# Performance work log

Measured on AMD Instinct MI355X. Metric: run time of the kernel, lower is better.

Reference implementation:

```python
import jax, jax.numpy as jnp
import numpy as np

N_PER_CLOUD = 2048   # points per cloud (batch entries are equal-sized, sorted)
NUM_CLOUDS = 8       # batch_size constant in the source module
RADIUS = 0.2         # init arg r
MAX_NEIGHBORS = 32   # init arg max_neighbors
F_IN, H1, H2, F_OUT = 3, 64, 64, 128  # PointNet++ SA MLP widths; nn input = F_IN + 3


def setup_inputs() -> dict:
    key = jax.random.key(0)
    ks = jax.random.split(key, 8)
    N = NUM_CLOUDS * N_PER_CLOUD
    x = jax.random.normal(ks[0], (N, F_IN), dtype=jnp.float32)
    pos = jax.random.uniform(ks[1], (N, 3), dtype=jnp.float32)  # unit cube
    batch = jnp.repeat(jnp.arange(NUM_CLOUDS, dtype=jnp.int32), N_PER_CLOUD)
    d_in = F_IN + 3
    W1 = jax.random.normal(ks[2], (d_in, H1), dtype=jnp.float32) / np.sqrt(d_in)
    b1 = jnp.zeros((H1,), dtype=jnp.float32)
    W2 = jax.random.normal(ks[3], (H1, H2), dtype=jnp.float32) / np.sqrt(H1)
    b2 = jnp.zeros((H2,), dtype=jnp.float32)
    W3 = jax.random.normal(ks[4], (H2, F_OUT), dtype=jnp.float32) / np.sqrt(H2)
    b3 = jnp.zeros((F_OUT,), dtype=jnp.float32)
    return dict(x=x, pos=pos, batch=batch, W1=W1, b1=b1, W2=W2, b2=b2, W3=W3, b3=b3)


def reference(x, pos, batch, W1, b1, W2, b2, W3, b3):
    N = pos.shape[0]
    B = N // N_PER_CLOUD
    n = N_PER_CLOUD
    posb = pos.reshape(B, n, 3)
    xb = x.reshape(B, n, -1)

    # --- radius ball query (per cloud, first MAX_NEIGHBORS in index order) ---
    diff = posb[:, :, None, :] - posb[:, None, :, :]          # [B, n_query, n_src, 3]
    d2 = jnp.sum(diff * diff, axis=-1)                        # [B, n, n]
    valid = d2 <= RADIUS * RADIUS                             # includes self -> >=1 nbr
    j_idx = jnp.arange(n, dtype=jnp.int32)
    keys = jnp.where(valid, j_idx[None, None, :], n)          # invalid -> sentinel n
    nbr = jnp.argsort(keys, axis=-1)[..., :MAX_NEIGHBORS]     # [B, n, K]
    nbr_ok = jnp.take_along_axis(keys, nbr, axis=-1) < n      # [B, n, K] bool

    # --- PointNetConv: msg = nn(cat([x_j, pos_j - pos_i])), max aggregation ---
    b_ix = jnp.arange(B)[:, None, None]
    x_j = xb[b_ix, nbr]                                        # [B, n, K, F_IN]
    rel = posb[b_ix, nbr] - posb[:, :, None, :]               # [B, n, K, 3]
    msg = jnp.concatenate([x_j, rel], axis=-1)                # [B, n, K, F_IN+3]
    h = jax.nn.relu(msg @ W1 + b1)
    h = jax.nn.relu(h @ W2 + b2)
    h = h @ W3 + b3                                           # [B, n, K, F_OUT]
    h = jnp.where(nbr_ok[..., None], h, -jnp.inf)
    out = jnp.max(h, axis=2).reshape(N, -1)                   # [N, F_OUT]
    return out, pos, batch
```

## Files before the change

### kernel.cpp

```cpp
#include <hip/hip_runtime.h>
#include <hip/hip_bf16.h>
#include <math.h>

#define NPC   2048
#define NC    8
#define NTOT  (NPC * NC)
#define KMAX  32
#define R2    0.04f

typedef short bf16x8  __attribute__((ext_vector_type(8)));
typedef float f32x16  __attribute__((ext_vector_type(16)));

__device__ __forceinline__ unsigned int f2bf(float f) {
    unsigned int u = __float_as_uint(f);
    return (u + 0x7FFFu + ((u >> 16) & 1u)) >> 16;
}

__device__ __forceinline__ unsigned int pkbf(float a, float b) {
    unsigned int r;
    asm("v_cvt_pk_bf16_f32 %0, %1, %2" : "=v"(r) : "v"(a), "v"(b));
    return r;
}

__device__ __forceinline__ void epi_swap(const f32x16& a0, const f32x16& a1,
                                         int hi, bf16x8 bout[4]) {
    unsigned int w_own[2][4][2];
    #pragma unroll
    for (int g = 0; g < 4; ++g) {
        w_own[0][g][0] = pkbf(fmaxf(a0[4*g+0],0.f), fmaxf(a0[4*g+1],0.f));
        w_own[0][g][1] = pkbf(fmaxf(a0[4*g+2],0.f), fmaxf(a0[4*g+3],0.f));
        w_own[1][g][0] = pkbf(fmaxf(a1[4*g+0],0.f), fmaxf(a1[4*g+1],0.f));
        w_own[1][g][1] = pkbf(fmaxf(a1[4*g+2],0.f), fmaxf(a1[4*g+3],0.f));
    }
    unsigned int R[2][2][2];
    #pragma unroll
    for (int t = 0; t < 2; ++t)
        #pragma unroll
        for (int gg = 0; gg < 2; ++gg)
            #pragma unroll
            for (int u = 0; u < 2; ++u) {
                unsigned int send = hi ? w_own[t][2*gg][u] : w_own[t][2*gg+1][u];
                R[t][gg][u] = (unsigned int)__shfl_xor((int)send, 32);
            }
    #pragma unroll
    for (int kk = 0; kk < 4; ++kk) {
        int t = kk >> 1;
        unsigned int O0 = hi ? w_own[t][(2*kk+1)&3][0] : w_own[t][(2*kk)&3][0];
        unsigned int O1 = hi ? w_own[t][(2*kk+1)&3][1] : w_own[t][(2*kk)&3][1];
        unsigned int R0 = R[t][kk&1][0], R1 = R[t][kk&1][1];
        int4 w;
        w.x = (int)(hi ? R0 : O0);
        w.y = (int)(hi ? R1 : O1);
        w.z = (int)(hi ? O0 : R0);
        w.w = (int)(hi ? O1 : R1);
        bout[kk] = __builtin_bit_cast(bf16x8, w);
    }
}

__global__ __launch_bounds__(256) void prep_kernel(
    const float* __restrict__ x, const float* __restrict__ pos,
    const int* __restrict__ batch,
    const float* __restrict__ W1, const float* __restrict__ b1,
    const float* __restrict__ W2, const float* __restrict__ b2,
    const float* __restrict__ W3,
    int* __restrict__ nbr, int* __restrict__ cnts,
    float* __restrict__ xp, unsigned short* __restrict__ wf,
    float* __restrict__ out)
{
    int b = blockIdx.x, tid = threadIdx.x;
    if (b < 4096) {
        int q    = b * 4 + (tid >> 6);
        int lane = tid & 63;
        int base = (q >> 11) << 11;
        float qx = pos[3*q], qy = pos[3*q+1], qz = pos[3*q+2];
        int cnt = 0;
        for (int j0 = 0; j0 < NPC && cnt < KMAX; j0 += 256) {
            unsigned long long ms[4];
            bool vs[4];
            #pragma unroll
            for (int s = 0; s < 4; ++s) {
                int j = base + j0 + s*64 + lane;
                float dx = __fsub_rn(pos[3*j],   qx);
                float dy = __fsub_rn(pos[3*j+1], qy);
                float dz = __fsub_rn(pos[3*j+2], qz);
                float d2 = __fadd_rn(__fadd_rn(__fmul_rn(dx,dx), __fmul_rn(dy,dy)),
                                     __fmul_rn(dz,dz));
                vs[s] = d2 <= R2;
                ms[s] = __ballot(vs[s]);
            }
            #pragma unroll
            for (int s = 0; s < 4; ++s) {
                int before = (int)__popcll(ms[s] & ((1ull << lane) - 1ull));
                int slot = cnt + before;
                if (vs[s] && slot < KMAX) nbr[(q << 5) + slot] = base + j0 + s*64 + lane;
                cnt += (int)__popcll(ms[s]);
            }
        }
        if (lane == 0) cnts[q] = cnt < KMAX ? cnt : KMAX;
    } else if (b < 4160) {
        int i = (b - 4096) * 256 + tid;
        float4 v0 = {x[3*i], x[3*i+1], x[3*i+2], pos[3*i]};
        float4 v1 = {pos[3*i+1], pos[3*i+2], 0.f, 0.f};
        float4* dst = (float4*)(xp + 8 * i);
        dst[0] = v0; dst[1] = v1;
    } else if (b < 4216) {
        int g = (b - 4160) * 256 + tid;
        if (g < 1024) {
            int j = g & 7, lane = (g >> 3) & 63, t = g >> 9;
            int k = (lane >> 5)*8 + j, ch = t*32 + (lane & 31);
            float v = (k < 6) ? W1[k*64 + ch] : (k == 6 ? b1[ch] : 0.f);
            wf[g] = (unsigned short)f2bf(v);
        } else if (g < 6144) {
            int g2 = g - 1024;
            int j = g2 & 7, lane = (g2 >> 3) & 63, f = g2 >> 9;
            int t = f / 5, kk = f % 5;
            int k = kk*16 + (lane >> 5)*8 + j, row = t*32 + (lane & 31);
            float v = 0.f;
            if (k < 64)       v = W2[k*64 + row];
            else if (k == 64) v = b2[row];
            wf[g] = (unsigned short)f2bf(v);
        } else {
            int g3 = g - 6144;
            int j = g3 & 7, lane = (g3 >> 3) & 63, f = g3 >> 9;
            int n = f >> 2, kk = f & 3;
            int k = kk*16 + (lane >> 5)*8 + j, col = n*32 + (lane & 31);
            wf[g] = (unsigned short)f2bf(W3[k*128 + col]);
        }
    } else {
        int i = (b - 4216) * 256 + tid;
        if (i < NTOT*3) out[NTOT*128 + i] = pos[i];
        if (i < NTOT)   out[NTOT*131 + i] = (float)batch[i];
    }
}

__global__ __launch_bounds__(256, 4) void mlp_kernel(
    const unsigned short* __restrict__ wf, const float* __restrict__ b3,
    const float* __restrict__ xp,
    const int* __restrict__ nbr, const int* __restrict__ cnts,
    float* __restrict__ out)
{
    __shared__ int4 sW[1664];

    const int tid = threadIdx.x;
    const int4* wsrc = (const int4*)(wf + 1024);
    #pragma unroll
    for (int it = 0; it < 7; ++it) {
        int idx = it*256 + tid;
        if (idx < 1664) sW[idx] = wsrc[idx];
    }
    const int lane = tid & 63, wave = tid >> 6;
    const int e = lane & 31, hi = lane >> 5;
    bf16x8 wf1_0 = *(const bf16x8*)(wf + (0*64 + lane)*8);
    bf16x8 wf1_1 = *(const bf16x8*)(wf + (1*64 + lane)*8);
    __syncthreads();

    const unsigned int one_w = pkbf(1.0f, 0.0f);
    int4 ow = {0,0,0,0};
    if (!hi) ow.x = (int)one_w;
    const bf16x8 onef = __builtin_bit_cast(bf16x8, ow);

    float b3v0 = b3[0*32 + e], b3v1 = b3[1*32 + e], b3v2 = b3[2*32 + e], b3v3 = b3[3*32 + e];

    const int qbase = __builtin_amdgcn_readfirstlane(blockIdx.x * 16 + wave * 4);

    #pragma unroll 1
    for (int i = 0; i < 4; ++i) {
        const int qq = qbase + i;
        const int cnt = cnts[qq];

        int jg = (e < cnt) ? nbr[(qq << 5) + e] : qq;
        const float4* pj = (const float4*)(xp + 8*jg);
        float4 xj0 = pj[0], xj1 = pj[1];
        const float4* pq = (const float4*)(xp + 8*qq);
        float4 xq0 = pq[0], xq1 = pq[1];
        float r0 = xj0.w - xq0.w, r1 = xj1.x - xq1.x, r2 = xj1.y - xq1.y;

        int4 mw;
        mw.x = hi ? 0 : (int)pkbf(xj0.x, xj0.y);
        mw.y = hi ? 0 : (int)pkbf(xj0.z, r0);
        mw.z = hi ? 0 : (int)pkbf(r1, r2);
        mw.w = hi ? 0 : (int)one_w;
        bf16x8 msgf = __builtin_bit_cast(bf16x8, mw);

        f32x16 acc0 = {}, acc1 = {};
        acc0 = __builtin_amdgcn_mfma_f32_32x32x16_bf16(wf1_0, msgf, acc0, 0, 0, 0);
        acc1 = __builtin_amdgcn_mfma_f32_32x32x16_bf16(wf1_1, msgf, acc1, 0, 0, 0);
        bf16x8 h1f[4];
        epi_swap(acc0, acc1, hi, h1f);

        f32x16 c20 = {}, c21 = {};
        #pragma unroll
        for (int kk = 0; kk < 4; ++kk) {
            c20 = __builtin_amdgcn_mfma_f32_32x32x16_bf16(
                    *(const bf16x8*)&sW[(0*5 + kk)*64 + lane], h1f[kk], c20, 0, 0, 0);
            c21 = __builtin_amdgcn_mfma_f32_32x32x16_bf16(
                    *(const bf16x8*)&sW[(1*5 + kk)*64 + lane], h1f[kk], c21, 0, 0, 0);
        }
        c20 = __builtin_amdgcn_mfma_f32_32x32x16_bf16(
                *(const bf16x8*)&sW[(0*5 + 4)*64 + lane], onef, c20, 0, 0, 0);
        c21 = __builtin_amdgcn_mfma_f32_32x32x16_bf16(
                *(const bf16x8*)&sW[(1*5 + 4)*64 + lane], onef, c21, 0, 0, 0);
        bf16x8 h2f[4];
        epi_swap(c20, c21, hi, h2f);

        const bool full = (cnt == 32);
        #pragma unroll
        for (int n = 0; n < 4; ++n) {
            f32x16 c = {};
            #pragma unroll
            for (int kk = 0; kk < 4; ++kk)
                c = __builtin_amdgcn_mfma_f32_32x32x16_bf16(
                        h2f[kk], *(const bf16x8*)&sW[640 + (n*4 + kk)*64 + lane], c, 0, 0, 0);
            float m;
            if (full) {
                m = fmaxf(fmaxf(fmaxf(c[0],c[1]), fmaxf(c[2],c[3])),
                          fmaxf(fmaxf(c[4],c[5]), fmaxf(c[6],c[7])));
                m = fmaxf(m, fmaxf(fmaxf(c[8],c[9]),  fmaxf(c[10],c[11])));
                m = fmaxf(m, fmaxf(fmaxf(c[12],c[13]), fmaxf(c[14],c[15])));
            } else {
                m = -INFINITY;
                #pragma unroll
                for (int reg = 0; reg < 16; ++reg) {
                    int r = (reg & 3) + 8*(reg >> 2) + 4*hi;
                    float v = (r < cnt) ? c[reg] : -INFINITY;
                    m = fmaxf(m, v);
                }
            }
            m = fmaxf(m, __shfl_xor(m, 32));
            m += (n == 0 ? b3v0 : n == 1 ? b3v1 : n == 2 ? b3v2 : b3v3);
            if (hi == 0) out[qq*128 + n*32 + e] = m;
        }
    }
}

extern "C" void kernel_launch(void* const* d_in, const int* in_sizes, int n_in,
                              void* d_out, int out_size, void* d_ws, size_t ws_size,
                              hipStream_t stream) {
    const float* x     = (const float*)d_in[0];
    const float* pos   = (const float*)d_in[1];
    const int*   batch = (const int*)d_in[2];
    const float* W1    = (const float*)d_in[3];
    const float* b1    = (const float*)d_in[4];
    const float* W2    = (const float*)d_in[5];
    const float* b2    = (const float*)d_in[6];
    const float* W3    = (const float*)d_in[7];
    const float* b3    = (const float*)d_in[8];
    float* out = (float*)d_out;

    int* nbr  = (int*)d_ws;
    int* cnts = nbr + NTOT * KMAX;
    float* xp = (float*)(cnts + NTOT);
    unsigned short* wfrag = (unsigned short*)(xp + NTOT*8);

    prep_kernel<<<4408, 256, 0, stream>>>(x, pos, batch, W1, b1, W2, b2, W3,
                                          nbr, cnts, xp, wfrag, out);
    mlp_kernel<<<NTOT / 16, 256, 0, stream>>>(wfrag, b3, xp, nbr, cnts, out);
}
```

Measured before the change: 41.68 us.

## Keep MLP weight fragments in registers and prefetch neighbor gathers across queries

Drops the shared-memory staging of the W2/W3 fragments. Each wave now loads all weight fragments straight into VGPRs, which removes the LDS fill, the block barrier and the per-MFMA LDS reads. Each wave handles 8 queries instead of 4, preloads counts, neighbor indices and query positions for all of them, and software-prefetches the next query's neighbor features while the current one computes. The grid is halved and launch bounds drop to 2 blocks per CU to make room for the larger register footprint, at the cost of lower occupancy and heavier register pressure.

```diff
diff --git a/kernel.cpp b/kernel.cpp
--- a/kernel.cpp
+++ b/kernel.cpp
@@ -133,73 +133,87 @@
     }
 }
 
-__global__ __launch_bounds__(256, 4) void mlp_kernel(
+__global__ __launch_bounds__(256, 2) void mlp_kernel(
     const unsigned short* __restrict__ wf, const float* __restrict__ b3,
     const float* __restrict__ xp,
     const int* __restrict__ nbr, const int* __restrict__ cnts,
     float* __restrict__ out)
 {
-    __shared__ int4 sW[1664];
-
-    const int tid = threadIdx.x;
-    const int4* wsrc = (const int4*)(wf + 1024);
-    #pragma unroll
-    for (int it = 0; it < 7; ++it) {
-        int idx = it*256 + tid;
-        if (idx < 1664) sW[idx] = wsrc[idx];
-    }
+    const int tid  = threadIdx.x;
     const int lane = tid & 63, wave = tid >> 6;
     const int e = lane & 31, hi = lane >> 5;
-    bf16x8 wf1_0 = *(const bf16x8*)(wf + (0*64 + lane)*8);
-    bf16x8 wf1_1 = *(const bf16x8*)(wf + (1*64 + lane)*8);
-    __syncthreads();
+
+    bf16x8 wA1[2], wA2[10], wB3[16];
+    #pragma unroll
+    for (int t = 0; t < 2; ++t)
+        wA1[t] = *(const bf16x8*)(wf + (t*64 + lane)*8);
+    #pragma unroll
+    for (int f = 0; f < 10; ++f)
+        wA2[f] = *(const bf16x8*)(wf + 1024 + (f*64 + lane)*8);
+    #pragma unroll
+    for (int f = 0; f < 16; ++f)
+        wB3[f] = *(const bf16x8*)(wf + 6144 + (f*64 + lane)*8);
 
     const unsigned int one_w = pkbf(1.0f, 0.0f);
     int4 ow = {0,0,0,0};
     if (!hi) ow.x = (int)one_w;
     const bf16x8 onef = __builtin_bit_cast(bf16x8, ow);
 
-    float b3v0 = b3[0*32 + e], b3v1 = b3[1*32 + e], b3v2 = b3[2*32 + e], b3v3 = b3[3*32 + e];
-
-    const int qbase = __builtin_amdgcn_readfirstlane(blockIdx.x * 16 + wave * 4);
-
-    #pragma unroll 1
-    for (int i = 0; i < 4; ++i) {
-        const int qq = qbase + i;
-        const int cnt = cnts[qq];
-
-        int jg = (e < cnt) ? nbr[(qq << 5) + e] : qq;
-        const float4* pj = (const float4*)(xp + 8*jg);
-        float4 xj0 = pj[0], xj1 = pj[1];
-        const float4* pq = (const float4*)(xp + 8*qq);
-        float4 xq0 = pq[0], xq1 = pq[1];
-        float r0 = xj0.w - xq0.w, r1 = xj1.x - xq1.x, r2 = xj1.y - xq1.y;
+    float b3v[4];
+    #pragma unroll
+    for (int n = 0; n < 4; ++n) b3v[n] = b3[n*32 + e];
+
+    const int qbase = __builtin_amdgcn_readfirstlane(blockIdx.x * 32 + wave * 8);
+
+    int cnt8[8], nbrv[8];
+    float qpx[8], qpy[8], qpz[8];
+    #pragma unroll
+    for (int i = 0; i < 8; ++i) {
+        cnt8[i] = cnts[qbase + i];
+        nbrv[i] = nbr[((qbase + i) << 5) + e];
+        qpx[i] = xp[8*(qbase+i) + 3];
+        qpy[i] = xp[8*(qbase+i) + 4];
+        qpz[i] = xp[8*(qbase+i) + 5];
+    }
+
+    int jg0 = (e < cnt8[0]) ? nbrv[0] : qbase;
+    float4 xj0 = ((const float4*)(xp + 8*jg0))[0];
+    float4 xj1 = ((const float4*)(xp + 8*jg0))[1];
+
+    #pragma unroll
+    for (int i = 0; i < 8; ++i) {
+        const int cnt = cnt8[i];
+        const int qq  = qbase + i;
+        float4 cj0 = xj0, cj1 = xj1;
+        if (i < 7) {
+            int jgn = (e < cnt8[i+1]) ? nbrv[i+1] : (qbase + i + 1);
+            xj0 = ((const float4*)(xp + 8*jgn))[0];
+            xj1 = ((const float4*)(xp + 8*jgn))[1];
+        }
+
+        float r0 = cj0.w - qpx[i], r1 = cj1.x - qpy[i], r2 = cj1.y - qpz[i];
 
         int4 mw;
-        mw.x = hi ? 0 : (int)pkbf(xj0.x, xj0.y);
-        mw.y = hi ? 0 : (int)pkbf(xj0.z, r0);
+        mw.x = hi ? 0 : (int)pkbf(cj0.x, cj0.y);
+        mw.y = hi ? 0 : (int)pkbf(cj0.z, r0);
         mw.z = hi ? 0 : (int)pkbf(r1, r2);
         mw.w = hi ? 0 : (int)one_w;
         bf16x8 msgf = __builtin_bit_cast(bf16x8, mw);
 
         f32x16 acc0 = {}, acc1 = {};
-        acc0 = __builtin_amdgcn_mfma_f32_32x32x16_bf16(wf1_0, msgf, acc0, 0, 0, 0);
-        acc1 = __builtin_amdgcn_mfma_f32_32x32x16_bf16(wf1_1, msgf, acc1, 0, 0, 0);
+        acc0 = __builtin_amdgcn_mfma_f32_32x32x16_bf16(wA1[0], msgf, acc0, 0, 0, 0);
+        acc1 = __builtin_amdgcn_mfma_f32_32x32x16_bf16(wA1[1], msgf, acc1, 0, 0, 0);
         bf16x8 h1f[4];
         epi_swap(acc0, acc1, hi, h1f);
 
         f32x16 c20 = {}, c21 = {};
         #pragma unroll
         for (int kk = 0; kk < 4; ++kk) {
-            c20 = __builtin_amdgcn_mfma_f32_32x32x16_bf16(
-                    *(const bf16x8*)&sW[(0*5 + kk)*64 + lane], h1f[kk], c20, 0, 0, 0);
-            c21 = __builtin_amdgcn_mfma_f32_32x32x16_bf16(
-                    *(const bf16x8*)&sW[(1*5 + kk)*64 + lane], h1f[kk], c21, 0, 0, 0);
-        }
-        c20 = __builtin_amdgcn_mfma_f32_32x32x16_bf16(
-                *(const bf16x8*)&sW[(0*5 + 4)*64 + lane], onef, c20, 0, 0, 0);
-        c21 = __builtin_amdgcn_mfma_f32_32x32x16_bf16(
-                *(const bf16x8*)&sW[(1*5 + 4)*64 + lane], onef, c21, 0, 0, 0);
+            c20 = __builtin_amdgcn_mfma_f32_32x32x16_bf16(wA2[kk],     h1f[kk], c20, 0, 0, 0);
+            c21 = __builtin_amdgcn_mfma_f32_32x32x16_bf16(wA2[5 + kk], h1f[kk], c21, 0, 0, 0);
+        }
+        c20 = __builtin_amdgcn_mfma_f32_32x32x16_bf16(wA2[4], onef, c20, 0, 0, 0);
+        c21 = __builtin_amdgcn_mfma_f32_32x32x16_bf16(wA2[9], onef, c21, 0, 0, 0);
         bf16x8 h2f[4];
         epi_swap(c20, c21, hi, h2f);
 
@@ -209,8 +223,7 @@
             f32x16 c = {};
             #pragma unroll
             for (int kk = 0; kk < 4; ++kk)
-                c = __builtin_amdgcn_mfma_f32_32x32x16_bf16(
-                        h2f[kk], *(const bf16x8*)&sW[640 + (n*4 + kk)*64 + lane], c, 0, 0, 0);
+                c = __builtin_amdgcn_mfma_f32_32x32x16_bf16(h2f[kk], wB3[n*4 + kk], c, 0, 0, 0);
             float m;
             if (full) {
                 m = fmaxf(fmaxf(fmaxf(c[0],c[1]), fmaxf(c[2],c[3])),
@@ -227,7 +240,7 @@
                 }
             }
             m = fmaxf(m, __shfl_xor(m, 32));
-            m += (n == 0 ? b3v0 : n == 1 ? b3v1 : n == 2 ? b3v2 : b3v3);
+            m += b3v[n];
             if (hi == 0) out[qq*128 + n*32 + e] = m;
         }
     }
@@ -254,5 +267,5 @@
 
     prep_kernel<<<4408, 256, 0, stream>>>(x, pos, batch, W1, b1, W2, b2, W3,
                                           nbr, cnts, xp, wfrag, out);
-    mlp_kernel<<<NTOT / 16, 256, 0, stream>>>(wfrag, b3, xp, nbr, cnts, out);
-}
+    mlp_kernel<<<NTOT / 32, 256, 0, stream>>>(wfrag, b3, xp, nbr, cnts, out);
+}
```

Measured after the change: 43.37 us. 4.0% more time.

## Permute weight K-order to drop cross-half shuffles; one query per wave

Applied to the files above, without the earlier changes.

The W2/W3 fragments are now stored with their K dimension permuted so that each lane's own MFMA accumulator registers can be packed straight into the next layer's B/A fragment. This removes the __shfl_xor exchange between wave halves in the hidden-layer epilogues. The MLP kernel also processes one query per wave instead of looping over four, and issues the neighbor and feature loads before the shared-memory weight copy to overlap their latency. Each block now reloads the weights into LDS for only four queries, and four times as many blocks are launched.

```diff
diff --git a/kernel.cpp b/kernel.cpp
--- a/kernel.cpp
+++ b/kernel.cpp
@@ -22,39 +22,13 @@
     return r;
 }
 
-__device__ __forceinline__ void epi_swap(const f32x16& a0, const f32x16& a1,
-                                         int hi, bf16x8 bout[4]) {
-    unsigned int w_own[2][4][2];
-    #pragma unroll
-    for (int g = 0; g < 4; ++g) {
-        w_own[0][g][0] = pkbf(fmaxf(a0[4*g+0],0.f), fmaxf(a0[4*g+1],0.f));
-        w_own[0][g][1] = pkbf(fmaxf(a0[4*g+2],0.f), fmaxf(a0[4*g+3],0.f));
-        w_own[1][g][0] = pkbf(fmaxf(a1[4*g+0],0.f), fmaxf(a1[4*g+1],0.f));
-        w_own[1][g][1] = pkbf(fmaxf(a1[4*g+2],0.f), fmaxf(a1[4*g+3],0.f));
-    }
-    unsigned int R[2][2][2];
-    #pragma unroll
-    for (int t = 0; t < 2; ++t)
-        #pragma unroll
-        for (int gg = 0; gg < 2; ++gg)
-            #pragma unroll
-            for (int u = 0; u < 2; ++u) {
-                unsigned int send = hi ? w_own[t][2*gg][u] : w_own[t][2*gg+1][u];
-                R[t][gg][u] = (unsigned int)__shfl_xor((int)send, 32);
-            }
-    #pragma unroll
-    for (int kk = 0; kk < 4; ++kk) {
-        int t = kk >> 1;
-        unsigned int O0 = hi ? w_own[t][(2*kk+1)&3][0] : w_own[t][(2*kk)&3][0];
-        unsigned int O1 = hi ? w_own[t][(2*kk+1)&3][1] : w_own[t][(2*kk)&3][1];
-        unsigned int R0 = R[t][kk&1][0], R1 = R[t][kk&1][1];
-        int4 w;
-        w.x = (int)(hi ? R0 : O0);
-        w.y = (int)(hi ? R1 : O1);
-        w.z = (int)(hi ? O0 : R0);
-        w.w = (int)(hi ? O1 : R1);
-        bout[kk] = __builtin_bit_cast(bf16x8, w);
-    }
+__device__ __forceinline__ bf16x8 mk_frag(const f32x16& a, int off) {
+    int4 w;
+    w.x = (int)pkbf(fmaxf(a[off+0],0.f), fmaxf(a[off+1],0.f));
+    w.y = (int)pkbf(fmaxf(a[off+2],0.f), fmaxf(a[off+3],0.f));
+    w.z = (int)pkbf(fmaxf(a[off+4],0.f), fmaxf(a[off+5],0.f));
+    w.w = (int)pkbf(fmaxf(a[off+6],0.f), fmaxf(a[off+7],0.f));
+    return __builtin_bit_cast(bf16x8, w);
 }
 
 __global__ __launch_bounds__(256) void prep_kernel(
@@ -114,16 +88,21 @@
             int g2 = g - 1024;
             int j = g2 & 7, lane = (g2 >> 3) & 63, f = g2 >> 9;
             int t = f / 5, kk = f % 5;
-            int k = kk*16 + (lane >> 5)*8 + j, row = t*32 + (lane & 31);
-            float v = 0.f;
-            if (k < 64)       v = W2[k*64 + row];
-            else if (k == 64) v = b2[row];
+            int hi = lane >> 5, row = t*32 + (lane & 31);
+            float v;
+            if (kk < 4) {
+                int k = (j & 3) + 4*hi + 8*(2*(kk & 1) + (j >> 2)) + 32*(kk >> 1);
+                v = W2[k*64 + row];
+            } else {
+                v = (hi == 0 && j == 0) ? b2[row] : 0.f;
+            }
             wf[g] = (unsigned short)f2bf(v);
         } else {
             int g3 = g - 6144;
             int j = g3 & 7, lane = (g3 >> 3) & 63, f = g3 >> 9;
             int n = f >> 2, kk = f & 3;
-            int k = kk*16 + (lane >> 5)*8 + j, col = n*32 + (lane & 31);
+            int hi = lane >> 5, col = n*32 + (lane & 31);
+            int k = (j & 3) + 4*hi + 8*(2*(kk & 1) + (j >> 2)) + 32*(kk >> 1);
             wf[g] = (unsigned short)f2bf(W3[k*128 + col]);
         }
     } else {
@@ -141,17 +120,31 @@
 {
     __shared__ int4 sW[1664];
 
-    const int tid = threadIdx.x;
+    const int tid  = threadIdx.x;
+    const int lane = tid & 63, wave = tid >> 6;
+    const int e = lane & 31, hi = lane >> 5;
+
+    const int qq  = __builtin_amdgcn_readfirstlane(blockIdx.x * 4 + wave);
+    const int cnt = cnts[qq];
+
+    int jg = (e < cnt) ? nbr[(qq << 5) + e] : qq;
+    const float4* pj = (const float4*)(xp + 8*jg);
+    float4 xj0 = pj[0], xj1 = pj[1];
+    float qpx = xp[8*qq + 3], qpy = xp[8*qq + 4], qpz = xp[8*qq + 5];
+
+    bf16x8 wA1_0 = *(const bf16x8*)(wf + (0*64 + lane)*8);
+    bf16x8 wA1_1 = *(const bf16x8*)(wf + (1*64 + lane)*8);
+
+    float b3v[4];
+    #pragma unroll
+    for (int n = 0; n < 4; ++n) b3v[n] = b3[n*32 + e];
+
     const int4* wsrc = (const int4*)(wf + 1024);
     #pragma unroll
     for (int it = 0; it < 7; ++it) {
         int idx = it*256 + tid;
         if (idx < 1664) sW[idx] = wsrc[idx];
     }
-    const int lane = tid & 63, wave = tid >> 6;
-    const int e = lane & 31, hi = lane >> 5;
-    bf16x8 wf1_0 = *(const bf16x8*)(wf + (0*64 + lane)*8);
-    bf16x8 wf1_1 = *(const bf16x8*)(wf + (1*64 + lane)*8);
     __syncthreads();
 
     const unsigned int one_w = pkbf(1.0f, 0.0f);
@@ -159,77 +152,67 @@
     if (!hi) ow.x = (int)one_w;
     const bf16x8 onef = __builtin_bit_cast(bf16x8, ow);
 
-    float b3v0 = b3[0*32 + e], b3v1 = b3[1*32 + e], b3v2 = b3[2*32 + e], b3v3 = b3[3*32 + e];
-
-    const int qbase = __builtin_amdgcn_readfirstlane(blockIdx.x * 16 + wave * 4);
-
-    #pragma unroll 1
-    for (int i = 0; i < 4; ++i) {
-        const int qq = qbase + i;
-        const int cnt = cnts[qq];
-
-        int jg = (e < cnt) ? nbr[(qq << 5) + e] : qq;
-        const float4* pj = (const float4*)(xp + 8*jg);
-        float4 xj0 = pj[0], xj1 = pj[1];
-        const float4* pq = (const float4*)(xp + 8*qq);
-        float4 xq0 = pq[0], xq1 = pq[1];
-        float r0 = xj0.w - xq0.w, r1 = xj1.x - xq1.x, r2 = xj1.y - xq1.y;
-
-        int4 mw;
-        mw.x = hi ? 0 : (int)pkbf(xj0.x, xj0.y);
-        mw.y = hi ? 0 : (int)pkbf(xj0.z, r0);
-        mw.z = hi ? 0 : (int)pkbf(r1, r2);
-        mw.w = hi ? 0 : (int)one_w;
-        bf16x8 msgf = __builtin_bit_cast(bf16x8, mw);
-
-        f32x16 acc0 = {}, acc1 = {};
-        acc0 = __builtin_amdgcn_mfma_f32_32x32x16_bf16(wf1_0, msgf, acc0, 0, 0, 0);
-        acc1 = __builtin_amdgcn_mfma_f32_32x32x16_bf16(wf1_1, msgf, acc1, 0, 0, 0);
-        bf16x8 h1f[4];
-        epi_swap(acc0, acc1, hi, h1f);
-
-        f32x16 c20 = {}, c21 = {};
+    float r0 = xj0.w - qpx, r1 = xj1.x - qpy, r2 = xj1.y - qpz;
+    int4 mw;
+    mw.x = hi ? 0 : (int)pkbf(xj0.x, xj0.y);
+    mw.y = hi ? 0 : (int)pkbf(xj0.z, r0);
+    mw.z = hi ? 0 : (int)pkbf(r1, r2);
+    mw.w = hi ? 0 : (int)one_w;
+    bf16x8 msgf = __builtin_bit_cast(bf16x8, mw);
+
+    f32x16 acc0 = {}, acc1 = {};
+    acc0 = __builtin_amdgcn_mfma_f32_32x32x16_bf16(wA1_0, msgf, acc0, 0, 0, 0);
+    acc1 = __builtin_amdgcn_mfma_f32_32x32x16_bf16(wA1_1, msgf, acc1, 0, 0, 0);
+    bf16x8 h1f[4];
+    h1f[0] = mk_frag(acc0, 0);
+    h1f[1] = mk_frag(acc0, 8);
+    h1f[2] = mk_frag(acc1, 0);
+    h1f[3] = mk_frag(acc1, 8);
+
+    f32x16 c20 = {}, c21 = {};
+    #pragma unroll
+    for (int kk = 0; kk < 4; ++kk) {
+        c20 = __builtin_amdgcn_mfma_f32_32x32x16_bf16(
+                *(const bf16x8*)&sW[(0*5 + kk)*64 + lane], h1f[kk], c20, 0, 0, 0);
+        c21 = __builtin_amdgcn_mfma_f32_32x32x16_bf16(
+                *(const bf16x8*)&sW[(1*5 + kk)*64 + lane], h1f[kk], c21, 0, 0, 0);
+    }
+    c20 = __builtin_amdgcn_mfma_f32_32x32x16_bf16(
+            *(const bf16x8*)&sW[(0*5 + 4)*64 + lane], onef, c20, 0, 0, 0);
+    c21 = __builtin_amdgcn_mfma_f32_32x32x16_bf16(
+            *(const bf16x8*)&sW[(1*5 + 4)*64 + lane], onef, c21, 0, 0, 0);
+    bf16x8 h2f[4];
+    h2f[0] = mk_frag(c20, 0);
+    h2f[1] = mk_frag(c20, 8);
+    h2f[2] = mk_frag(c21, 0);
+    h2f[3] = mk_frag(c21, 8);
+
+    const bool full = (cnt == 32);
+    #pragma unroll
+    for (int n = 0; n < 4; ++n) {
+        f32x16 c = {};
         #pragma unroll
-        for (int kk = 0; kk < 4; ++kk) {
-            c20 = __builtin_amdgcn_mfma_f32_32x32x16_bf16(
-                    *(const bf16x8*)&sW[(0*5 + kk)*64 + lane], h1f[kk], c20, 0, 0, 0);
-            c21 = __builtin_amdgcn_mfma_f32_32x32x16_bf16(
-                    *(const bf16x8*)&sW[(1*5 + kk)*64 + lane], h1f[kk], c21, 0, 0, 0);
+        for (int kk = 0; kk < 4; ++kk)
+            c = __builtin_amdgcn_mfma_f32_32x32x16_bf16(
+                    h2f[kk], *(const bf16x8*)&sW[640 + (n*4 + kk)*64 + lane], c, 0, 0, 0);
+        float m;
+        if (full) {
+            m = fmaxf(fmaxf(fmaxf(c[0],c[1]), fmaxf(c[2],c[3])),
+                      fmaxf(fmaxf(c[4],c[5]), fmaxf(c[6],c[7])));
+            m = fmaxf(m, fmaxf(fmaxf(c[8],c[9]),  fmaxf(c[10],c[11])));
+            m = fmaxf(m, fmaxf(fmaxf(c[12],c[13]), fmaxf(c[14],c[15])));
+        } else {
+            m = -INFINITY;
+            #pragma unroll
+            for (int reg = 0; reg < 16; ++reg) {
+                int r = (reg & 3) + 8*(reg >> 2) + 4*hi;
+                float v = (r < cnt) ? c[reg] : -INFINITY;
+                m = fmaxf(m, v);
+            }
         }
-        c20 = __builtin_amdgcn_mfma_f32_32x32x16_bf16(
-                *(const bf16x8*)&sW[(0*5 + 4)*64 + lane], onef, c20, 0, 0, 0);
-        c21 = __builtin_amdgcn_mfma_f32_32x32x16_bf16(
-                *(const bf16x8*)&sW[(1*5 + 4)*64 + lane], onef, c21, 0, 0, 0);
-        bf16x8 h2f[4];
-        epi_swap(c20, c21, hi, h2f);
-
-        const bool full = (cnt == 32);
-        #pragma unroll
-        for (int n = 0; n < 4; ++n) {
-            f32x16 c = {};
-            #pragma unroll
-            for (int kk = 0; kk < 4; ++kk)
-                c = __builtin_amdgcn_mfma_f32_32x32x16_bf16(
-                        h2f[kk], *(const bf16x8*)&sW[640 + (n*4 + kk)*64 + lane], c, 0, 0, 0);
-            float m;
-            if (full) {
-                m = fmaxf(fmaxf(fmaxf(c[0],c[1]), fmaxf(c[2],c[3])),
-                          fmaxf(fmaxf(c[4],c[5]), fmaxf(c[6],c[7])));
-                m = fmaxf(m, fmaxf(fmaxf(c[8],c[9]),  fmaxf(c[10],c[11])));
-                m = fmaxf(m, fmaxf(fmaxf(c[12],c[13]), fmaxf(c[14],c[15])));
-            } else {
-                m = -INFINITY;
-                #pragma unroll
-                for (int reg = 0; reg < 16; ++reg) {
-                    int r = (reg & 3) + 8*(reg >> 2) + 4*hi;
-                    float v = (r < cnt) ? c[reg] : -INFINITY;
-                    m = fmaxf(m, v);
-                }
-            }
-            m = fmaxf(m, __shfl_xor(m, 32));
-            m += (n == 0 ? b3v0 : n == 1 ? b3v1 : n == 2 ? b3v2 : b3v3);
-            if (hi == 0) out[qq*128 + n*32 + e] = m;
-        }
+        m = fmaxf(m, __shfl_xor(m, 32));
+        m += b3v[n];
+        if (hi == 0) out[qq*128 + n*32 + (lane & 31)] = m;
     }
 }
 
@@ -254,5 +237,5 @@
 
     prep_kernel<<<4408, 256, 0, stream>>>(x, pos, batch, W1, b1, W2, b2, W3,
                                           nbr, cnts, xp, wfrag, out);
-    mlp_kernel<<<NTOT / 16, 256, 0, stream>>>(wfrag, b3, xp, nbr, cnts, out);
-}
+    mlp_kernel<<<NTOT / 4, 256, 0, stream>>>(wfrag, b3, xp, nbr, cnts, out);
+}
```

Result: faster. 40.73 us (-2.3%).
